# Performance work log

Measured on AMD Instinct MI355X. Metric: run time of the kernel, lower is better.

Reference implementation:

```python
import jax, jax.numpy as jnp
import numpy as np

EMBED = 1024
HEADS = 16
DH = EMBED // HEADS
B, S = 2, 2048


def setup_inputs() -> dict:
    key = jax.random.key(0)
    ks = jax.random.split(key, 12)
    inp = {
        "k": jax.random.normal(ks[0], (B, S, EMBED), jnp.float32),
        "q": jax.random.normal(ks[1], (B, S, EMBED), jnp.float32),
        "v": jax.random.normal(ks[2], (B, S, EMBED), jnp.float32),
        "mask": jax.random.randint(ks[3], (B, 1, S, S), 0, 2, jnp.int32),
        # per-head projections (shared across heads, as in the torch module)
        "Wk": jax.random.normal(ks[4], (DH, DH), jnp.float32) / np.sqrt(DH),
        "bk": jnp.zeros((DH,), jnp.float32),
        "Wq": jax.random.normal(ks[5], (DH, DH), jnp.float32) / np.sqrt(DH),
        "bq": jnp.zeros((DH,), jnp.float32),
        "Wv": jax.random.normal(ks[6], (DH, DH), jnp.float32) / np.sqrt(DH),
        "bv": jnp.zeros((DH,), jnp.float32),
        "Wo": jax.random.normal(ks[7], (EMBED, EMBED), jnp.float32) / np.sqrt(EMBED),
        "bo": jnp.zeros((EMBED,), jnp.float32),
    }
    return inp


def reference(k, q, v, mask, Wk, bk, Wq, bq, Wv, bv, Wo, bo):
    b, s, _ = k.shape
    sq = q.shape[1]
    # [B,S,H,dh]
    kh = k.reshape(b, s, HEADS, DH)
    qh = q.reshape(b, sq, HEADS, DH)
    vh = v.reshape(b, s, HEADS, DH)
    # per-head linear (weight shared across heads): x @ W.T + b
    kh = kh @ Wk.T + bk
    qh = qh @ Wq.T + bq
    vh = vh @ Wv.T + bv
    # scores [B,H,Sq,Sk]
    product = jnp.einsum("bqhd,bkhd->bhqk", qh, kh)
    # masked_fill BEFORE scaling, as in the original
    product = jnp.where(mask == 0, jnp.float32(-1e20), product)
    product = product / np.sqrt(DH)
    scores = jax.nn.softmax(product, axis=-1)
    ctx = jnp.einsum("bhqk,bkhd->bqhd", scores, vh).reshape(b, sq, EMBED)
    return ctx @ Wo.T + bo
```

## Files before the change

### kernel.cpp

```cpp
#include <hip/hip_runtime.h>
#include <hip/hip_bf16.h>
#include <math.h>

#define EMBED 1024
#define HEADS 16
#define DH    64
#define BATCH 2
#define SEQ   2048

typedef __attribute__((ext_vector_type(8))) short bf16x8;
typedef __attribute__((ext_vector_type(4))) short bf16x4;
typedef __attribute__((ext_vector_type(4))) float f32x4;
typedef unsigned long long u64;

#define QSCALE 0.1803368801111244f

static __device__ __forceinline__ unsigned short f2bf(float x) {
    unsigned u = __builtin_bit_cast(unsigned, x);
    return (unsigned short)((u + 0x7fffu + ((u >> 16) & 1u)) >> 16);
}
static __device__ __forceinline__ unsigned pk2bf(float a, float b) {
    union { __hip_bfloat162 h2; unsigned u; } c;
    c.h2 = __float22bfloat162_rn(make_float2(a, b));
    return c.u;
}
static __device__ __forceinline__ void gl_lds16(const void* g, void* l) {
    __builtin_amdgcn_global_load_lds(
        (const __attribute__((address_space(1))) void*)g,
        (__attribute__((address_space(3))) void*)l, 16, 0, 0);
}
static __device__ __forceinline__ bf16x8 cvt8(const float* p) {
    float4 a = ((const float4*)p)[0];
    float4 b = ((const float4*)p)[1];
    union { unsigned u[4]; bf16x8 v; } c;
    c.u[0] = pk2bf(a.x, a.y); c.u[1] = pk2bf(a.z, a.w);
    c.u[2] = pk2bf(b.x, b.y); c.u[3] = pk2bf(b.z, b.w);
    return c.v;
}

__global__ __launch_bounds__(256) void proj_mfma(
    const float* __restrict__ q, const float* __restrict__ k, const float* __restrict__ v,
    const float* __restrict__ Wq, const float* __restrict__ bq,
    const float* __restrict__ Wk, const float* __restrict__ bk,
    const float* __restrict__ Wv, const float* __restrict__ bv,
    unsigned short* __restrict__ qh, unsigned short* __restrict__ kh,
    unsigned short* __restrict__ vh)
{
    const int blk = blockIdx.x;
    const int which = blockIdx.y;
    const float* x; const float* W; const float* bias; unsigned short* out;
    if (which == 0)      { x = q; W = Wq; bias = bq; out = qh; }
    else if (which == 1) { x = k; W = Wk; bias = bk; out = kh; }
    else                 { x = v; W = Wv; bias = bv; out = vh; }
    const float oscale = (which == 0) ? QSCALE : 1.0f;

    __shared__ unsigned short Ws[64 * 72];

    const int t    = threadIdx.x;
    const int w    = t >> 6;
    const int lane = t & 63;
    const int l15  = lane & 15;
    const int quad = lane >> 4;

    const int sr = t >> 2, sp = t & 3;
    {
        const float* wsrc = W + (size_t)sr * 64 + sp * 16;
        unsigned o32[8];
#pragma unroll
        for (int u4 = 0; u4 < 4; ++u4) {
            float4 a = ((const float4*)wsrc)[u4];
            o32[u4 * 2 + 0] = pk2bf(a.x, a.y);
            o32[u4 * 2 + 1] = pk2bf(a.z, a.w);
        }
        *(uint4*)&Ws[sr * 72 + sp * 16]     = *(uint4*)&o32[0];
        *(uint4*)&Ws[sr * 72 + sp * 16 + 8] = *(uint4*)&o32[4];
    }

    const float* xrow = x + ((size_t)blk * 64 + w * 16 + l15) * 64;
    const bf16x8 af0 = cvt8(xrow + quad * 8);
    const bf16x8 af1 = cvt8(xrow + 32 + quad * 8);

    __syncthreads();

    f32x4 acc[4];
#pragma unroll
    for (int nt = 0; nt < 4; ++nt) {
        bf16x8 bf0 = *(const bf16x8*)&Ws[(nt * 16 + l15) * 72 + quad * 8];
        bf16x8 bf1 = *(const bf16x8*)&Ws[(nt * 16 + l15) * 72 + 32 + quad * 8];
        f32x4 a = {0, 0, 0, 0};
        a = __builtin_amdgcn_mfma_f32_16x16x32_bf16(af0, bf0, a, 0, 0, 0);
        a = __builtin_amdgcn_mfma_f32_16x16x32_bf16(af1, bf1, a, 0, 0, 0);
        acc[nt] = a;
    }

    const int bsidx = blk * 4 + w;
    const int b = bsidx >> 11, s = bsidx & 2047;
#pragma unroll
    for (int nt = 0; nt < 4; ++nt) {
        const int d = nt * 16 + l15;
        const float bb = bias[d];
#pragma unroll
        for (int r = 0; r < 4; ++r) {
            const int h = quad * 4 + r;
            out[(((size_t)b * HEADS + h) * SEQ + s) * DH + d] =
                f2bf((acc[nt][r] + bb) * oscale);
        }
    }
}

__global__ __launch_bounds__(256) void prep_kernel(
    const unsigned short* __restrict__ vh, unsigned short* __restrict__ vt,
    const int* __restrict__ mask, u64* __restrict__ bits,
    const float* __restrict__ Wo, unsigned short* __restrict__ Wob)
{
    __shared__ unsigned short Tt[64 * 72];
    const int bid = blockIdx.x;
    const int t   = threadIdx.x;

    if (bid < 1024) {
        const int st = bid & 31;
        const int bh = bid >> 5;
        const int r = t >> 2, p = t & 3;
        const unsigned short* src = vh + ((size_t)bh * SEQ + st * 64 + r) * DH + p * 16;
        *(uint4*)&Tt[r * 72 + p * 16]     = *(const uint4*)src;
        *(uint4*)&Tt[r * 72 + p * 16 + 8] = *(const uint4*)(src + 8);
        __syncthreads();
        union { unsigned short u[16]; uint4 v[2]; } o;
#pragma unroll
        for (int u = 0; u < 16; ++u) o.u[u] = Tt[(p * 16 + u) * 72 + r];
        unsigned short* dst = vt + ((size_t)bh * DH + r) * SEQ + st * 64 + p * 16;
        *(uint4*)dst       = o.v[0];
        *(uint4*)(dst + 8) = o.v[1];
    } else if (bid < 1536) {
        const int idx = (bid - 1024) * 256 + t;
        const int4* src = (const int4*)(mask + (size_t)idx * 64);
        u64 w = 0;
#pragma unroll
        for (int u = 0; u < 16; ++u) {
            int4 m = src[u];
            u64 nib = (m.x != 0 ? 1ull : 0) | (m.y != 0 ? 2ull : 0) |
                      (m.z != 0 ? 4ull : 0) | (m.w != 0 ? 8ull : 0);
            w |= nib << (u * 4);
        }
        bits[idx] = w;
    } else {
        const int i = ((bid - 1536) * 256 + t) * 8;
        float4 a = ((const float4*)(Wo + i))[0];
        float4 b = ((const float4*)(Wo + i))[1];
        unsigned o32[4] = {pk2bf(a.x, a.y), pk2bf(a.z, a.w),
                           pk2bf(b.x, b.y), pk2bf(b.z, b.w)};
        *(uint4*)(Wob + i) = *(uint4*)o32;
    }
}

__global__ __launch_bounds__(256, 4) void attn_kernel(
    const unsigned short* __restrict__ qh, const unsigned short* __restrict__ kh,
    const unsigned short* __restrict__ vt, const u64* __restrict__ mbits,
    unsigned short* __restrict__ ctx)
{
    const int bid = blockIdx.x;
    const int bh  = bid & 31;
    const int q0  = (bid >> 5) * 64;
    const int b   = bh >> 4;

    __shared__ unsigned char smem[32768];

    const int t    = threadIdx.x;
    const int w    = t >> 6;
    const int lane = t & 63;
    const int l15  = lane & 15;
    const int quad = lane >> 4;

    const int srow   = lane >> 3;
    const int schunk = (lane & 7) ^ srow;

    const unsigned short* qb = qh + ((size_t)bh * SEQ + q0 + w * 16 + l15) * DH + quad * 8;
    const bf16x8 qf0 = *(const bf16x8*)qb;
    const bf16x8 qf1 = *(const bf16x8*)(qb + 32);

    f32x4 O[4];
#pragma unroll
    for (int dt = 0; dt < 4; ++dt) O[dt] = f32x4{0, 0, 0, 0};
    f32x4 Osum = {0, 0, 0, 0};
    const bf16x4 ones = {(short)0x3F80, (short)0x3F80, (short)0x3F80, (short)0x3F80};

    const unsigned short* kbase = kh + (size_t)bh * SEQ * DH
                                  + (size_t)srow * DH + schunk * 8;
    const unsigned short* vbase = vt + (size_t)bh * DH * SEQ
                                  + (size_t)srow * SEQ + schunk * 8;
    const u64* mrow = mbits + ((size_t)b * SEQ + q0 + w * 16 + l15) * (SEQ / 64);

    if (w < 2) {
        unsigned char* Kd = smem;
#pragma unroll
        for (int j = 0; j < 4; ++j) {
            const int i = w * 4 + j;
            gl_lds16(kbase + (size_t)i * 8 * DH, Kd + i * 1024);
        }
    } else {
        unsigned char* Vd = smem + 8192;
#pragma unroll
        for (int j = 0; j < 4; ++j) {
            const int i = (w - 2) * 4 + j;
            gl_lds16(vbase + (size_t)i * 8 * SEQ, Vd + i * 1024);
        }
    }
    u64 pm = mrow[0];
    __syncthreads();

    for (int kt = 0; kt < 32; ++kt) {
        if (kt < 31) {
            const int bn = (kt + 1) & 1;
            if (w < 2) {
                unsigned char* Kd = smem + bn * 16384;
                const unsigned short* g0 = kbase + (size_t)(kt + 1) * 64 * DH;
#pragma unroll
                for (int j = 0; j < 4; ++j) {
                    const int i = w * 4 + j;
                    gl_lds16(g0 + (size_t)i * 8 * DH, Kd + i * 1024);
                }
            } else {
                unsigned char* Vd = smem + bn * 16384 + 8192;
                const unsigned short* g0 = vbase + (kt + 1) * 64;
#pragma unroll
                for (int j = 0; j < 4; ++j) {
                    const int i = (w - 2) * 4 + j;
                    gl_lds16(g0 + (size_t)i * 8 * SEQ, Vd + i * 1024);
                }
            }
        }
        const u64 mb = pm;
        if (kt < 31) pm = mrow[kt + 1];

        const unsigned short* KtH = (const unsigned short*)(smem + (kt & 1) * 16384);
        const unsigned short* VtH = KtH + 4096;

        const u64 mq = mb >> (quad * 4);
        bf16x4 p[4];
        const int rx = l15 & 7;
#pragma unroll
        for (int st = 0; st < 4; ++st) {
            const int r = st * 16 + l15;
            bf16x8 kf0 = *(const bf16x8*)&KtH[r * 64 + ((quad ^ rx)) * 8];
            bf16x8 kf1 = *(const bf16x8*)&KtH[r * 64 + ((quad ^ rx) ^ 4) * 8];
            f32x4 sa = {0, 0, 0, 0};
            sa = __builtin_amdgcn_mfma_f32_16x16x32_bf16(kf0, qf0, sa, 0, 0, 0);
            sa = __builtin_amdgcn_mfma_f32_16x16x32_bf16(kf1, qf1, sa, 0, 0, 0);
            const unsigned nib = (unsigned)(mq >> (st * 16)) & 0xFu;
            float p0 = (nib & 1u) ? exp2f(sa[0]) : 0.f;
            float p1 = (nib & 2u) ? exp2f(sa[1]) : 0.f;
            float p2 = (nib & 4u) ? exp2f(sa[2]) : 0.f;
            float p3 = (nib & 8u) ? exp2f(sa[3]) : 0.f;
            union { unsigned u2[2]; bf16x4 v; } pu;
            pu.u2[0] = pk2bf(p0, p1);
            pu.u2[1] = pk2bf(p2, p3);
            p[st] = pu.v;
            Osum = __builtin_amdgcn_mfma_f32_16x16x16bf16_1k(p[st], ones, Osum, 0, 0, 0);
        }

#pragma unroll
        for (int dt = 0; dt < 4; ++dt) {
            const int d = dt * 16 + l15;
            const int dx = l15 & 7;
#pragma unroll
            for (int st = 0; st < 4; ++st) {
                const int ch = (st * 2 + (quad >> 1)) ^ dx;
                bf16x4 vb = *(const bf16x4*)&VtH[d * 64 + ch * 8 + (quad & 1) * 4];
                O[dt] = __builtin_amdgcn_mfma_f32_16x16x16bf16_1k(p[st], vb, O[dt], 0, 0, 0);
            }
        }
        __syncthreads();
    }

    float inv[4];
#pragma unroll
    for (int r = 0; r < 4; ++r) inv[r] = 1.0f / Osum[r];
#pragma unroll
    for (int r = 0; r < 4; ++r) {
        const int row = q0 + w * 16 + quad * 4 + r;
        unsigned short* dst = ctx + ((size_t)bh * SEQ + row) * DH + l15;
#pragma unroll
        for (int dt = 0; dt < 4; ++dt)
            dst[dt * 16] = f2bf(O[dt][r] * inv[r]);
    }
}

__global__ __launch_bounds__(256, 4) void outproj_mfma(
    const unsigned short* __restrict__ ctx, const unsigned short* __restrict__ Wob,
    const float* __restrict__ bo, float* __restrict__ out)
{
    const int n0 = blockIdx.x * 64;
    const int m0 = blockIdx.y * 64;
    const int b  = m0 / SEQ;
    const int s0 = m0 % SEQ;

    __shared__ unsigned char smem[32768];

    const int t    = threadIdx.x;
    const int w    = t >> 6;
    const int lane = t & 63;
    const int l15  = lane & 15;
    const int quad = lane >> 4;
    const int srow   = lane >> 3;
    const int schunk = (lane & 7) ^ srow;

    const unsigned short* abase = ctx + ((size_t)b * HEADS * SEQ + s0 + srow) * DH + schunk * 8;
    const unsigned short* wbase = Wob + (size_t)(n0 + srow) * EMBED + schunk * 8;

    f32x4 acc[4] = {f32x4{0,0,0,0}, f32x4{0,0,0,0}, f32x4{0,0,0,0}, f32x4{0,0,0,0}};

    {
        unsigned char* Ab = smem;
        unsigned char* Wb = smem + 8192;
#pragma unroll
        for (int j = 0; j < 4; ++j) {
            const int idx = w * 4 + j;
            if (idx < 8)
                gl_lds16(abase + (size_t)idx * 8 * DH, Ab + idx * 1024);
            else
                gl_lds16(wbase + (size_t)(idx - 8) * 8 * EMBED, Wb + (idx - 8) * 1024);
        }
    }
    __syncthreads();

    for (int kt = 0; kt < 16; ++kt) {
        if (kt < 15) {
            const int ktn = kt + 1;
            unsigned char* Ab = smem + (ktn & 1) * 16384;
            unsigned char* Wb = Ab + 8192;
#pragma unroll
            for (int j = 0; j < 4; ++j) {
                const int idx = w * 4 + j;
                if (idx < 8)
                    gl_lds16(abase + (size_t)ktn * SEQ * DH + (size_t)idx * 8 * DH,
                             Ab + idx * 1024);
                else
                    gl_lds16(wbase + (size_t)(idx - 8) * 8 * EMBED + ktn * 64,
                             Wb + (idx - 8) * 1024);
            }
        }

        const unsigned short* At = (const unsigned short*)(smem + (kt & 1) * 16384);
        const unsigned short* Wt = At + 4096;
        const int rx = l15 & 7;
        const int c0 = ((quad ^ rx)) * 8;

        bf16x8 bf0 = *(const bf16x8*)&Wt[(w * 16 + l15) * 64 + c0];
        bf16x8 bf1 = *(const bf16x8*)&Wt[(w * 16 + l15) * 64 + (c0 ^ 32)];
#pragma unroll
        for (int mt = 0; mt < 4; ++mt) {
            bf16x8 af0 = *(const bf16x8*)&At[(mt * 16 + l15) * 64 + c0];
            bf16x8 af1 = *(const bf16x8*)&At[(mt * 16 + l15) * 64 + (c0 ^ 32)];
            acc[mt] = __builtin_amdgcn_mfma_f32_16x16x32_bf16(af0, bf0, acc[mt], 0, 0, 0);
            acc[mt] = __builtin_amdgcn_mfma_f32_16x16x32_bf16(af1, bf1, acc[mt], 0, 0, 0);
        }
        __syncthreads();
    }

    const float bv = bo[n0 + w * 16 + l15];
#pragma unroll
    for (int mt = 0; mt < 4; ++mt) {
#pragma unroll
        for (int r = 0; r < 4; ++r) {
            out[(size_t)(m0 + mt * 16 + quad * 4 + r) * EMBED + n0 + w * 16 + l15] =
                acc[mt][r] + bv;
        }
    }
}

extern "C" void kernel_launch(void* const* d_in, const int* in_sizes, int n_in,
                              void* d_out, int out_size, void* d_ws, size_t ws_size,
                              hipStream_t stream) {
    const float* k    = (const float*)d_in[0];
    const float* q    = (const float*)d_in[1];
    const float* v    = (const float*)d_in[2];
    const int*   mask = (const int*)  d_in[3];
    const float* Wk   = (const float*)d_in[4];
    const float* bk   = (const float*)d_in[5];
    const float* Wq   = (const float*)d_in[6];
    const float* bq   = (const float*)d_in[7];
    const float* Wv   = (const float*)d_in[8];
    const float* bv   = (const float*)d_in[9];
    const float* Wo   = (const float*)d_in[10];
    const float* bo   = (const float*)d_in[11];
    float* out = (float*)d_out;

    const size_t TEN = (size_t)BATCH * HEADS * SEQ * DH;
    unsigned short* qh_bf = (unsigned short*)d_ws;
    unsigned short* kh_bf = qh_bf + TEN;
    unsigned short* vh_bf = kh_bf + TEN;
    unsigned short* vt_bf = vh_bf + TEN;
    unsigned short* ctxb  = vt_bf + TEN;
    unsigned short* Wob   = ctxb + TEN;
    u64*            mbits = (u64*)(Wob + EMBED * EMBED);

    proj_mfma<<<dim3(BATCH * SEQ * HEADS / 64, 3), 256, 0, stream>>>(
        q, k, v, Wq, bq, Wk, bk, Wv, bv, qh_bf, kh_bf, vh_bf);
    prep_kernel<<<dim3(2048), 256, 0, stream>>>(
        vh_bf, vt_bf, mask, mbits, Wo, Wob);
    attn_kernel<<<dim3((SEQ / 64) * BATCH * HEADS), 256, 0, stream>>>(
        qh_bf, kh_bf, vt_bf, mbits, ctxb);
    outproj_mfma<<<dim3(EMBED / 64, BATCH * SEQ / 64), 256, 0, stream>>>(
        ctxb, Wob, bo, out);
}
```

Baseline: 240.0 us.

## Fuse V transpose, mask packing and Wo conversion into projection kernel

Removes the separate prep kernel. The V projection now computes Wv·x^T with MFMA so it writes the transposed V layout directly, with no intermediate vh buffer or shared-memory transpose. Mask bit-packing and Wo bf16 conversion run as extra blocks (y=3) of the projection launch. This saves one launch and a round trip of V through global memory, at the cost of scattered 2-byte transposed stores and idle blocks in the y=3 slice.

```diff
diff --git a/kernel.cpp b/kernel.cpp
--- a/kernel.cpp
+++ b/kernel.cpp
@@ -44,19 +44,45 @@
     const float* __restrict__ Wk, const float* __restrict__ bk,
     const float* __restrict__ Wv, const float* __restrict__ bv,
     unsigned short* __restrict__ qh, unsigned short* __restrict__ kh,
-    unsigned short* __restrict__ vh)
+    unsigned short* __restrict__ vt,
+    const int* __restrict__ mask, u64* __restrict__ bits,
+    const float* __restrict__ Wo, unsigned short* __restrict__ Wob)
 {
-    const int blk = blockIdx.x;
+    const int blk   = blockIdx.x;
     const int which = blockIdx.y;
-    const float* x; const float* W; const float* bias; unsigned short* out;
-    if (which == 0)      { x = q; W = Wq; bias = bq; out = qh; }
-    else if (which == 1) { x = k; W = Wk; bias = bk; out = kh; }
-    else                 { x = v; W = Wv; bias = bv; out = vh; }
-    const float oscale = (which == 0) ? QSCALE : 1.0f;
+    const int t     = threadIdx.x;
+
+    if (which == 3) {
+        if (blk < 512) {
+            const int idx = blk * 256 + t;
+            const int4* src = (const int4*)(mask + (size_t)idx * 64);
+            u64 wb = 0;
+#pragma unroll
+            for (int u = 0; u < 16; ++u) {
+                int4 m = src[u];
+                u64 nib = (m.x != 0 ? 1ull : 0) | (m.y != 0 ? 2ull : 0) |
+                          (m.z != 0 ? 4ull : 0) | (m.w != 0 ? 8ull : 0);
+                wb |= nib << (u * 4);
+            }
+            bits[idx] = wb;
+        } else {
+            const int i = ((blk - 512) * 256 + t) * 8;
+            float4 a = ((const float4*)(Wo + i))[0];
+            float4 b = ((const float4*)(Wo + i))[1];
+            unsigned o32[4] = {pk2bf(a.x, a.y), pk2bf(a.z, a.w),
+                               pk2bf(b.x, b.y), pk2bf(b.z, b.w)};
+            *(uint4*)(Wob + i) = *(uint4*)o32;
+        }
+        return;
+    }
+
+    const float* x; const float* W; const float* bias;
+    if (which == 0)      { x = q; W = Wq; bias = bq; }
+    else if (which == 1) { x = k; W = Wk; bias = bk; }
+    else                 { x = v; W = Wv; bias = bv; }
 
     __shared__ unsigned short Ws[64 * 72];
 
-    const int t    = threadIdx.x;
     const int w    = t >> 6;
     const int lane = t & 63;
     const int l15  = lane & 15;
@@ -75,6 +101,37 @@
         *(uint4*)&Ws[sr * 72 + sp * 16]     = *(uint4*)&o32[0];
         *(uint4*)&Ws[sr * 72 + sp * 16 + 8] = *(uint4*)&o32[4];
     }
+
+    if (which == 2) {
+        const int bh = blk >> 5;
+        const int st = blk & 31;
+        const int b  = bh >> 4, h = bh & 15;
+        const int s  = st * 64 + w * 16 + l15;
+
+        const float* xrow = x + ((size_t)(b * SEQ + s)) * EMBED + h * DH;
+        const bf16x8 bx0 = cvt8(xrow + quad * 8);
+        const bf16x8 bx1 = cvt8(xrow + 32 + quad * 8);
+
+        __syncthreads();
+
+#pragma unroll
+        for (int nt = 0; nt < 4; ++nt) {
+            bf16x8 aw0 = *(const bf16x8*)&Ws[(nt * 16 + l15) * 72 + quad * 8];
+            bf16x8 aw1 = *(const bf16x8*)&Ws[(nt * 16 + l15) * 72 + 32 + quad * 8];
+            f32x4 a = {0, 0, 0, 0};
+            a = __builtin_amdgcn_mfma_f32_16x16x32_bf16(aw0, bx0, a, 0, 0, 0);
+            a = __builtin_amdgcn_mfma_f32_16x16x32_bf16(aw1, bx1, a, 0, 0, 0);
+#pragma unroll
+            for (int r = 0; r < 4; ++r) {
+                const int d = nt * 16 + quad * 4 + r;
+                vt[((size_t)bh * DH + d) * SEQ + s] = f2bf(a[r] + bias[d]);
+            }
+        }
+        return;
+    }
+
+    const float oscale = (which == 0) ? QSCALE : 1.0f;
+    unsigned short* out = (which == 0) ? qh : kh;
 
     const float* xrow = x + ((size_t)blk * 64 + w * 16 + l15) * 64;
     const bf16x8 af0 = cvt8(xrow + quad * 8);
@@ -105,51 +162,6 @@
             out[(((size_t)b * HEADS + h) * SEQ + s) * DH + d] =
                 f2bf((acc[nt][r] + bb) * oscale);
         }
-    }
-}
-
-__global__ __launch_bounds__(256) void prep_kernel(
-    const unsigned short* __restrict__ vh, unsigned short* __restrict__ vt,
-    const int* __restrict__ mask, u64* __restrict__ bits,
-    const float* __restrict__ Wo, unsigned short* __restrict__ Wob)
-{
-    __shared__ unsigned short Tt[64 * 72];
-    const int bid = blockIdx.x;
-    const int t   = threadIdx.x;
-
-    if (bid < 1024) {
-        const int st = bid & 31;
-        const int bh = bid >> 5;
-        const int r = t >> 2, p = t & 3;
-        const unsigned short* src = vh + ((size_t)bh * SEQ + st * 64 + r) * DH + p * 16;
-        *(uint4*)&Tt[r * 72 + p * 16]     = *(const uint4*)src;
-        *(uint4*)&Tt[r * 72 + p * 16 + 8] = *(const uint4*)(src + 8);
-        __syncthreads();
-        union { unsigned short u[16]; uint4 v[2]; } o;
-#pragma unroll
-        for (int u = 0; u < 16; ++u) o.u[u] = Tt[(p * 16 + u) * 72 + r];
-        unsigned short* dst = vt + ((size_t)bh * DH + r) * SEQ + st * 64 + p * 16;
-        *(uint4*)dst       = o.v[0];
-        *(uint4*)(dst + 8) = o.v[1];
-    } else if (bid < 1536) {
-        const int idx = (bid - 1024) * 256 + t;
-        const int4* src = (const int4*)(mask + (size_t)idx * 64);
-        u64 w = 0;
-#pragma unroll
-        for (int u = 0; u < 16; ++u) {
-            int4 m = src[u];
-            u64 nib = (m.x != 0 ? 1ull : 0) | (m.y != 0 ? 2ull : 0) |
-                      (m.z != 0 ? 4ull : 0) | (m.w != 0 ? 8ull : 0);
-            w |= nib << (u * 4);
-        }
-        bits[idx] = w;
-    } else {
-        const int i = ((bid - 1536) * 256 + t) * 8;
-        float4 a = ((const float4*)(Wo + i))[0];
-        float4 b = ((const float4*)(Wo + i))[1];
-        unsigned o32[4] = {pk2bf(a.x, a.y), pk2bf(a.z, a.w),
-                           pk2bf(b.x, b.y), pk2bf(b.z, b.w)};
-        *(uint4*)(Wob + i) = *(uint4*)o32;
     }
 }
 
@@ -388,16 +400,14 @@
     const size_t TEN = (size_t)BATCH * HEADS * SEQ * DH;
     unsigned short* qh_bf = (unsigned short*)d_ws;
     unsigned short* kh_bf = qh_bf + TEN;
-    unsigned short* vh_bf = kh_bf + TEN;
-    unsigned short* vt_bf = vh_bf + TEN;
+    unsigned short* vt_bf = kh_bf + TEN;
     unsigned short* ctxb  = vt_bf + TEN;
     unsigned short* Wob   = ctxb + TEN;
     u64*            mbits = (u64*)(Wob + EMBED * EMBED);
 
-    proj_mfma<<<dim3(BATCH * SEQ * HEADS / 64, 3), 256, 0, stream>>>(
-        q, k, v, Wq, bq, Wk, bk, Wv, bv, qh_bf, kh_bf, vh_bf);
-    prep_kernel<<<dim3(2048), 256, 0, stream>>>(
-        vh_bf, vt_bf, mask, mbits, Wo, Wob);
+    proj_mfma<<<dim3(1024, 4), 256, 0, stream>>>(
+        q, k, v, Wq, bq, Wk, bk, Wv, bv,
+        qh_bf, kh_bf, vt_bf, mask, mbits, Wo, Wob);
     attn_kernel<<<dim3((SEQ / 64) * BATCH * HEADS), 256, 0, stream>>>(
         qh_bf, kh_bf, vt_bf, mbits, ctxb);
     outproj_mfma<<<dim3(EMBED / 64, BATCH * SEQ / 64), 256, 0, stream>>>(
```

Measured after the change: 240.0 us. Within noise of the previous version (-0.0%).
